# Performance work log

Measured on AMD Instinct MI355X. Metric: run time of the kernel, lower is better.

## Reference

```python
import jax, jax.numpy as jnp
import numpy as np

T, D, E = 65536, 2048, 128
K, G, GLIM = 4, 2, 1  # top-k experts, expert groups, limited groups
TEMP = 1.0
ROUTE_SCALE = 1.0


def setup_inputs() -> dict:
    key = jax.random.key(0)
    kx, kw, kb = jax.random.split(key, 3)
    x = jax.random.normal(kx, (T, D), dtype=jnp.float32)
    # scale router weight so logits have O(1) std (module zero-inits; random here for a non-degenerate test)
    W = jax.random.normal(kw, (E, D), dtype=jnp.float32) * 0.02
    bias = jax.random.normal(kb, (E,), dtype=jnp.float32) * 0.01
    return {"x": x, "W": W, "bias": bias}


def reference(x, W, bias):
    Ttok = x.shape[0]
    gs = E // G  # group size
    logits = x @ W.T + bias                      # [T, E]
    scores = jax.nn.softmax(logits / max(TEMP, 1e-6), axis=-1)
    original_scores = scores
    # group-limited routing (bias is not None -> group rep = sum of top-2 in group)
    scores_g = scores.reshape(Ttok, G, gs)       # [T, G, gs]
    top2 = jax.lax.top_k(scores_g, 2)[0].sum(axis=-1)   # [T, G]
    grp_idx = jax.lax.top_k(top2, GLIM)[1]       # [T, g]
    allow_g = jnp.zeros((Ttok, G), dtype=bool).at[jnp.arange(Ttok)[:, None], grp_idx].set(True)
    allow = jnp.repeat(allow_g, gs, axis=1)      # [T, E]
    masked = jnp.where(allow_g[:, :, None], scores_g, -jnp.inf).reshape(Ttok, E)
    idx = jax.lax.top_k(masked, K)[1]            # [T, k] expert indices
    w = jnp.take_along_axis(original_scores, idx, axis=1)
    w = w / jnp.clip(w.sum(axis=-1, keepdims=True), 1e-9)
    if ROUTE_SCALE != 1.0:
        w = w * ROUTE_SCALE
    return w.astype(x.dtype), idx
```

## Files before the change

### kernel.cpp

```cpp
#include <hip/hip_runtime.h>
#include <math.h>

#define T_TOK 65536
#define D_DIM 2048
#define E_EXP 128
#define K_TOP 4
#define GS    64

#define BM   128
#define BK   32
#define NCH  (D_DIM / BK)
#define LROW 129

#define XSCALE 256.0f
#define WSCALE 256.0f
#define OSCALE (1.0f / 65536.0f)

#define WS_BYTES ((size_t)E_EXP * D_DIM * 2  * 2 )

typedef _Float16 f16x8 __attribute__((ext_vector_type(8)));
typedef float    f32x4 __attribute__((ext_vector_type(4)));
typedef unsigned short u16;

__device__ __forceinline__ void gload_lds16(const void* g, void* l) {
  __builtin_amdgcn_global_load_lds(
      (const __attribute__((address_space(1))) unsigned int*)g,
      (__attribute__((address_space(3))) unsigned int*)l, 16, 0, 0);
}

__global__ __launch_bounds__(256) void prep_w(const float* __restrict__ W,
                                              u16* __restrict__ wsB) {
  const int gid = blockIdx.x * 256 + threadIdx.x;
  const int e   = gid >> 8;
  const int k0  = (gid & 255) << 3;
  const int c   = k0 >> 5;
  const int ks  = (k0 >> 3) & 3;
  const int n16 = e >> 4, r16 = e & 15;
  const float* wp = W + (size_t)e * D_DIM + k0;
  float4 w0 = *(const float4*)(wp);
  float4 w1 = *(const float4*)(wp + 4);
  const float f[8] = {w0.x, w0.y, w0.z, w0.w, w1.x, w1.y, w1.z, w1.w};
  f16x8 hv, lv;
#pragma unroll
  for (int j = 0; j < 8; ++j) {
    float s = f[j] * WSCALE;
    _Float16 h = (_Float16)s;
    hv[j] = h;
    lv[j] = (_Float16)(s - (float)h);
  }
  u16* dst = wsB + (size_t)c * 8192 + (size_t)(n16 * 64 + ks * 16 + r16) * 8;
  *(f16x8*)(dst)        = hv;
  *(f16x8*)(dst + 4096) = lv;
}

template <bool USE_WS>
__global__ __launch_bounds__(256, 2) void gemm_gate(
    const float* __restrict__ x, const float* __restrict__ W,
    const u16* __restrict__ wsB, const float* __restrict__ bias,
    float* __restrict__ w_out, float* __restrict__ idx_out) {
  __shared__ __align__(16) unsigned char smem[BM * LROW * 4];
  __shared__ float bias_lds[E_EXP];
  u16*   As = (u16*)smem;
  u16*   Bs = (u16*)(smem + 16384);
  float* Ls = (float*)smem;

  const int tid = threadIdx.x;
  const int l   = tid & 63;
  const int wid = tid >> 6;
  const int wm  = wid >> 1;
  const int wn  = wid & 1;
  const int lu  = l * 8;

  if (tid < E_EXP) bias_lds[tid] = bias[tid];

  const int row = tid >> 1;
  const int kh  = tid & 1;
  const int m16 = row >> 4, r16 = row & 15;
  const int aw  = (m16 * 64 + kh * 32 + r16) * 8;
  const float* xp = x + (size_t)(blockIdx.x * BM + row) * D_DIM + kh * 16;
  const float* wp = W + (size_t)row * D_DIM + kh * 16;

  f32x4 acc[4][4], sh[4][4];
  const f32x4 vzero = {0.f, 0.f, 0.f, 0.f};
#pragma unroll
  for (int i = 0; i < 4; ++i)
#pragma unroll
    for (int j = 0; j < 4; ++j) { acc[i][j] = vzero; sh[i][j] = vzero; }

  float4 xv0 = *(const float4*)(xp);
  float4 xv1 = *(const float4*)(xp + 4);
  float4 xv2 = *(const float4*)(xp + 8);
  float4 xv3 = *(const float4*)(xp + 12);
  float4 wv0, wv1, wv2, wv3;
  if constexpr (!USE_WS) {
    wv0 = *(const float4*)(wp);
    wv1 = *(const float4*)(wp + 4);
    wv2 = *(const float4*)(wp + 8);
    wv3 = *(const float4*)(wp + 12);
  }

  for (int c = 0; c < NCH; ++c) {
    __syncthreads();

    {
      const float f[16] = {xv0.x, xv0.y, xv0.z, xv0.w, xv1.x, xv1.y, xv1.z, xv1.w,
                           xv2.x, xv2.y, xv2.z, xv2.w, xv3.x, xv3.y, xv3.z, xv3.w};
      f16x8 h0, h1, l0, l1;
#pragma unroll
      for (int j = 0; j < 8; ++j) {
        float sa = f[j] * XSCALE;
        _Float16 ha = (_Float16)sa;
        h0[j] = ha; l0[j] = (_Float16)(sa - (float)ha);
        float sb = f[j + 8] * XSCALE;
        _Float16 hb = (_Float16)sb;
        h1[j] = hb; l1[j] = (_Float16)(sb - (float)hb);
      }
      *(f16x8*)(As + aw)        = h0;
      *(f16x8*)(As + aw + 128)  = h1;
      *(f16x8*)(As + aw + 4096) = l0;
      *(f16x8*)(As + aw + 4224) = l1;
    }

    if constexpr (USE_WS) {
      const u16* src = wsB + (size_t)c * 8192 + tid * 8;
      u16* dst = Bs + tid * 8;
#pragma unroll
      for (int i = 0; i < 4; ++i)
        gload_lds16(src + i * 2048, dst + i * 2048);
    } else {
      const float f[16] = {wv0.x, wv0.y, wv0.z, wv0.w, wv1.x, wv1.y, wv1.z, wv1.w,
                           wv2.x, wv2.y, wv2.z, wv2.w, wv3.x, wv3.y, wv3.z, wv3.w};
      f16x8 h0, h1, l0, l1;
#pragma unroll
      for (int j = 0; j < 8; ++j) {
        float sa = f[j] * WSCALE;
        _Float16 ha = (_Float16)sa;
        h0[j] = ha; l0[j] = (_Float16)(sa - (float)ha);
        float sb = f[j + 8] * WSCALE;
        _Float16 hb = (_Float16)sb;
        h1[j] = hb; l1[j] = (_Float16)(sb - (float)hb);
      }
      *(f16x8*)(Bs + aw)        = h0;
      *(f16x8*)(Bs + aw + 128)  = h1;
      *(f16x8*)(Bs + aw + 4096) = l0;
      *(f16x8*)(Bs + aw + 4224) = l1;
    }

    __syncthreads();

    if (c + 1 < NCH) {
      const float* xn = xp + (c + 1) * 32;
      xv0 = *(const float4*)(xn);
      xv1 = *(const float4*)(xn + 4);
      xv2 = *(const float4*)(xn + 8);
      xv3 = *(const float4*)(xn + 12);
      if constexpr (!USE_WS) {
        const float* wn_ = wp + (c + 1) * 32;
        wv0 = *(const float4*)(wn_);
        wv1 = *(const float4*)(wn_ + 4);
        wv2 = *(const float4*)(wn_ + 8);
        wv3 = *(const float4*)(wn_ + 12);
      }
    }

    f16x8 Ah[4], Al[4];
#pragma unroll
    for (int m_ = 0; m_ < 4; ++m_) {
      const int mt = wm * 4 + m_;
      Ah[m_] = *(const f16x8*)(As + mt * 512 + lu);
      Al[m_] = *(const f16x8*)(As + 4096 + mt * 512 + lu);
    }
#pragma unroll
    for (int n_ = 0; n_ < 4; ++n_) {
      const int nt = wn * 4 + n_;
      f16x8 Bh = *(const f16x8*)(Bs + nt * 512 + lu);
      f16x8 Bl = *(const f16x8*)(Bs + 4096 + nt * 512 + lu);
#pragma unroll
      for (int m_ = 0; m_ < 4; ++m_) {
        acc[m_][n_] = __builtin_amdgcn_mfma_f32_16x16x32_f16(Ah[m_], Bh, acc[m_][n_], 0, 0, 0);
        acc[m_][n_] = __builtin_amdgcn_mfma_f32_16x16x32_f16(Ah[m_], Bl, acc[m_][n_], 0, 0, 0);
        acc[m_][n_] = __builtin_amdgcn_mfma_f32_16x16x32_f16(Al[m_], Bh, acc[m_][n_], 0, 0, 0);
      }
    }

    if ((c & 3) == 3) {
#pragma unroll
      for (int i = 0; i < 4; ++i)
#pragma unroll
        for (int j = 0; j < 4; ++j) { sh[i][j] += acc[i][j]; acc[i][j] = vzero; }
    }
  }

  __syncthreads();

#pragma unroll
  for (int m_ = 0; m_ < 4; ++m_) {
#pragma unroll
    for (int n_ = 0; n_ < 4; ++n_) {
      const int gcol  = wn * 64 + n_ * 16 + (l & 15);
      const int grow0 = wm * 64 + m_ * 16 + ((l >> 4) << 2);
#pragma unroll
      for (int q = 0; q < 4; ++q)
        Ls[(grow0 + q) * LROW + gcol] = sh[m_][n_][q] * OSCALE;
    }
  }
  __syncthreads();

  if (tid < BM) {
    const float* rowp = Ls + tid * LROW;

    float m1[2], m2[2];
#pragma unroll
    for (int g = 0; g < 2; ++g) {
      m1[g] = -INFINITY;
      m2[g] = -INFINITY;
      for (int e = 0; e < GS; ++e) {
        float v = rowp[g * GS + e] + bias_lds[g * GS + e];
        if (v > m1[g]) { m2[g] = m1[g]; m1[g] = v; }
        else if (v > m2[g]) { m2[g] = v; }
      }
    }
    float M  = fmaxf(m1[0], m1[1]);
    float r0 = expf(m1[0] - M) + expf(m2[0] - M);
    float r1 = expf(m1[1] - M) + expf(m2[1] - M);
    int g = (r1 > r0) ? 1 : 0;

    float v4[4] = {-INFINITY, -INFINITY, -INFINITY, -INFINITY};
    int i4[4] = {0, 0, 0, 0};
    const int base = g * GS;
    for (int e = 0; e < GS; ++e) {
      float v = rowp[base + e] + bias_lds[base + e];
      if (v > v4[3]) {
        if (v > v4[1]) {
          if (v > v4[0]) {
            v4[3] = v4[2]; i4[3] = i4[2];
            v4[2] = v4[1]; i4[2] = i4[1];
            v4[1] = v4[0]; i4[1] = i4[0];
            v4[0] = v; i4[0] = e;
          } else {
            v4[3] = v4[2]; i4[3] = i4[2];
            v4[2] = v4[1]; i4[2] = i4[1];
            v4[1] = v; i4[1] = e;
          }
        } else {
          if (v > v4[2]) {
            v4[3] = v4[2]; i4[3] = i4[2];
            v4[2] = v; i4[2] = e;
          } else {
            v4[3] = v; i4[3] = e;
          }
        }
      }
    }

    float s[4], sum = 0.0f;
#pragma unroll
    for (int j = 0; j < 4; ++j) { s[j] = expf(v4[j] - M); sum += s[j]; }
    float denom = fmaxf(sum, 1e-9f);
    const int t = blockIdx.x * BM + tid;
#pragma unroll
    for (int j = 0; j < 4; ++j) {
      w_out[(size_t)t * K_TOP + j]   = s[j] / denom;
      idx_out[(size_t)t * K_TOP + j] = (float)(base + i4[j]);
    }
  }
}

extern "C" void kernel_launch(void* const* d_in, const int* in_sizes, int n_in,
                              void* d_out, int out_size, void* d_ws, size_t ws_size,
                              hipStream_t stream) {
  (void)in_sizes; (void)n_in; (void)out_size;
  const float* x    = (const float*)d_in[0];
  const float* W    = (const float*)d_in[1];
  const float* bias = (const float*)d_in[2];
  float* out = (float*)d_out;

  const bool use_ws = (d_ws != nullptr) && (ws_size >= WS_BYTES);
  if (use_ws) {
    u16* wsB = (u16*)d_ws;
    prep_w<<<E_EXP, 256, 0, stream>>>(W, wsB);
    gemm_gate<true><<<T_TOK / BM, 256, 0, stream>>>(
        x, W, wsB, bias, out, out + (size_t)T_TOK * K_TOP);
  } else {
    gemm_gate<false><<<T_TOK / BM, 256, 0, stream>>>(
        x, W, nullptr, bias, out, out + (size_t)T_TOK * K_TOP);
  }
}
```

Before: 780.8 us.

## Double-buffer LDS tiles to overlap staging with MFMA compute

```diff
diff --git a/kernel.cpp b/kernel.cpp
--- a/kernel.cpp
+++ b/kernel.cpp
@@ -53,6 +53,51 @@
   *(f16x8*)(dst + 4096) = lv;
 }
 
+__device__ __forceinline__ void stage16(u16* dst, int aw, const float4& v0,
+                                        const float4& v1, const float4& v2,
+                                        const float4& v3, float scale) {
+  const float f[16] = {v0.x, v0.y, v0.z, v0.w, v1.x, v1.y, v1.z, v1.w,
+                       v2.x, v2.y, v2.z, v2.w, v3.x, v3.y, v3.z, v3.w};
+  f16x8 h0, h1, l0, l1;
+#pragma unroll
+  for (int j = 0; j < 8; ++j) {
+    float sa = f[j] * scale;
+    _Float16 ha = (_Float16)sa;
+    h0[j] = ha; l0[j] = (_Float16)(sa - (float)ha);
+    float sb = f[j + 8] * scale;
+    _Float16 hb = (_Float16)sb;
+    h1[j] = hb; l1[j] = (_Float16)(sb - (float)hb);
+  }
+  *(f16x8*)(dst + aw)        = h0;
+  *(f16x8*)(dst + aw + 128)  = h1;
+  *(f16x8*)(dst + aw + 4096) = l0;
+  *(f16x8*)(dst + aw + 4224) = l1;
+}
+
+__device__ __forceinline__ void compute32(const u16* As_, const u16* Bs_,
+                                          int wm, int wn, int lu,
+                                          f32x4 (&acc)[4][4]) {
+  f16x8 Ah[4], Al[4];
+#pragma unroll
+  for (int m_ = 0; m_ < 4; ++m_) {
+    const int mt = wm * 4 + m_;
+    Ah[m_] = *(const f16x8*)(As_ + mt * 512 + lu);
+    Al[m_] = *(const f16x8*)(As_ + 4096 + mt * 512 + lu);
+  }
+#pragma unroll
+  for (int n_ = 0; n_ < 4; ++n_) {
+    const int nt = wn * 4 + n_;
+    f16x8 Bh = *(const f16x8*)(Bs_ + nt * 512 + lu);
+    f16x8 Bl = *(const f16x8*)(Bs_ + 4096 + nt * 512 + lu);
+#pragma unroll
+    for (int m_ = 0; m_ < 4; ++m_) {
+      acc[m_][n_] = __builtin_amdgcn_mfma_f32_16x16x32_f16(Ah[m_], Bh, acc[m_][n_], 0, 0, 0);
+      acc[m_][n_] = __builtin_amdgcn_mfma_f32_16x16x32_f16(Ah[m_], Bl, acc[m_][n_], 0, 0, 0);
+      acc[m_][n_] = __builtin_amdgcn_mfma_f32_16x16x32_f16(Al[m_], Bh, acc[m_][n_], 0, 0, 0);
+    }
+  }
+}
+
 template <bool USE_WS>
 __global__ __launch_bounds__(256, 2) void gemm_gate(
     const float* __restrict__ x, const float* __restrict__ W,
@@ -60,8 +105,10 @@
     float* __restrict__ w_out, float* __restrict__ idx_out) {
   __shared__ __align__(16) unsigned char smem[BM * LROW * 4];
   __shared__ float bias_lds[E_EXP];
-  u16*   As = (u16*)smem;
-  u16*   Bs = (u16*)(smem + 16384);
+  u16* As0 = (u16*)smem;
+  u16* As1 = As0 + 8192;
+  u16* Bs0 = As0 + 16384;
+  u16* Bs1 = As0 + 24576;
   float* Ls = (float*)smem;
 
   const int tid = threadIdx.x;
@@ -87,111 +134,87 @@
 #pragma unroll
     for (int j = 0; j < 4; ++j) { acc[i][j] = vzero; sh[i][j] = vzero; }
 
-  float4 xv0 = *(const float4*)(xp);
-  float4 xv1 = *(const float4*)(xp + 4);
-  float4 xv2 = *(const float4*)(xp + 8);
-  float4 xv3 = *(const float4*)(xp + 12);
-  float4 wv0, wv1, wv2, wv3;
-  if constexpr (!USE_WS) {
-    wv0 = *(const float4*)(wp);
-    wv1 = *(const float4*)(wp + 4);
-    wv2 = *(const float4*)(wp + 8);
-    wv3 = *(const float4*)(wp + 12);
-  }
-
-  for (int c = 0; c < NCH; ++c) {
-    __syncthreads();
-
+  float4 xa0, xa1, xa2, xa3, xb0, xb1, xb2, xb3;
+  float4 wa0, wa1, wa2, wa3, wb0, wb1, wb2, wb3;
+
+  {
+    float4 t0 = *(const float4*)(xp);
+    float4 t1 = *(const float4*)(xp + 4);
+    float4 t2 = *(const float4*)(xp + 8);
+    float4 t3 = *(const float4*)(xp + 12);
+    stage16(As0, aw, t0, t1, t2, t3, XSCALE);
+    if constexpr (USE_WS) {
+      const u16* src = wsB + tid * 8;
+#pragma unroll
+      for (int i = 0; i < 4; ++i)
+        gload_lds16(src + i * 2048, Bs0 + tid * 8 + i * 2048);
+    } else {
+      float4 s0 = *(const float4*)(wp);
+      float4 s1 = *(const float4*)(wp + 4);
+      float4 s2 = *(const float4*)(wp + 8);
+      float4 s3 = *(const float4*)(wp + 12);
+      stage16(Bs0, aw, s0, s1, s2, s3, WSCALE);
+    }
+    const float* xn = xp + BK;
+    xb0 = *(const float4*)(xn);      xb1 = *(const float4*)(xn + 4);
+    xb2 = *(const float4*)(xn + 8);  xb3 = *(const float4*)(xn + 12);
+    if constexpr (!USE_WS) {
+      const float* wn_ = wp + BK;
+      wb0 = *(const float4*)(wn_);      wb1 = *(const float4*)(wn_ + 4);
+      wb2 = *(const float4*)(wn_ + 8);  wb3 = *(const float4*)(wn_ + 12);
+    }
+  }
+  __syncthreads();
+
+  for (int c = 0; c < NCH; c += 2) {
     {
-      const float f[16] = {xv0.x, xv0.y, xv0.z, xv0.w, xv1.x, xv1.y, xv1.z, xv1.w,
-                           xv2.x, xv2.y, xv2.z, xv2.w, xv3.x, xv3.y, xv3.z, xv3.w};
-      f16x8 h0, h1, l0, l1;
-#pragma unroll
-      for (int j = 0; j < 8; ++j) {
-        float sa = f[j] * XSCALE;
-        _Float16 ha = (_Float16)sa;
-        h0[j] = ha; l0[j] = (_Float16)(sa - (float)ha);
-        float sb = f[j + 8] * XSCALE;
-        _Float16 hb = (_Float16)sb;
-        h1[j] = hb; l1[j] = (_Float16)(sb - (float)hb);
-      }
-      *(f16x8*)(As + aw)        = h0;
-      *(f16x8*)(As + aw + 128)  = h1;
-      *(f16x8*)(As + aw + 4096) = l0;
-      *(f16x8*)(As + aw + 4224) = l1;
-    }
-
-    if constexpr (USE_WS) {
-      const u16* src = wsB + (size_t)c * 8192 + tid * 8;
-      u16* dst = Bs + tid * 8;
-#pragma unroll
-      for (int i = 0; i < 4; ++i)
-        gload_lds16(src + i * 2048, dst + i * 2048);
-    } else {
-      const float f[16] = {wv0.x, wv0.y, wv0.z, wv0.w, wv1.x, wv1.y, wv1.z, wv1.w,
-                           wv2.x, wv2.y, wv2.z, wv2.w, wv3.x, wv3.y, wv3.z, wv3.w};
-      f16x8 h0, h1, l0, l1;
-#pragma unroll
-      for (int j = 0; j < 8; ++j) {
-        float sa = f[j] * WSCALE;
-        _Float16 ha = (_Float16)sa;
-        h0[j] = ha; l0[j] = (_Float16)(sa - (float)ha);
-        float sb = f[j + 8] * WSCALE;
-        _Float16 hb = (_Float16)sb;
-        h1[j] = hb; l1[j] = (_Float16)(sb - (float)hb);
-      }
-      *(f16x8*)(Bs + aw)        = h0;
-      *(f16x8*)(Bs + aw + 128)  = h1;
-      *(f16x8*)(Bs + aw + 4096) = l0;
-      *(f16x8*)(Bs + aw + 4224) = l1;
-    }
-
-    __syncthreads();
-
-    if (c + 1 < NCH) {
-      const float* xn = xp + (c + 1) * 32;
-      xv0 = *(const float4*)(xn);
-      xv1 = *(const float4*)(xn + 4);
-      xv2 = *(const float4*)(xn + 8);
-      xv3 = *(const float4*)(xn + 12);
-      if constexpr (!USE_WS) {
-        const float* wn_ = wp + (c + 1) * 32;
-        wv0 = *(const float4*)(wn_);
-        wv1 = *(const float4*)(wn_ + 4);
-        wv2 = *(const float4*)(wn_ + 8);
-        wv3 = *(const float4*)(wn_ + 12);
-      }
-    }
-
-    f16x8 Ah[4], Al[4];
-#pragma unroll
-    for (int m_ = 0; m_ < 4; ++m_) {
-      const int mt = wm * 4 + m_;
-      Ah[m_] = *(const f16x8*)(As + mt * 512 + lu);
-      Al[m_] = *(const f16x8*)(As + 4096 + mt * 512 + lu);
-    }
-#pragma unroll
-    for (int n_ = 0; n_ < 4; ++n_) {
-      const int nt = wn * 4 + n_;
-      f16x8 Bh = *(const f16x8*)(Bs + nt * 512 + lu);
-      f16x8 Bl = *(const f16x8*)(Bs + 4096 + nt * 512 + lu);
-#pragma unroll
-      for (int m_ = 0; m_ < 4; ++m_) {
-        acc[m_][n_] = __builtin_amdgcn_mfma_f32_16x16x32_f16(Ah[m_], Bh, acc[m_][n_], 0, 0, 0);
-        acc[m_][n_] = __builtin_amdgcn_mfma_f32_16x16x32_f16(Ah[m_], Bl, acc[m_][n_], 0, 0, 0);
-        acc[m_][n_] = __builtin_amdgcn_mfma_f32_16x16x32_f16(Al[m_], Bh, acc[m_][n_], 0, 0, 0);
-      }
-    }
-
-    if ((c & 3) == 3) {
-#pragma unroll
-      for (int i = 0; i < 4; ++i)
-#pragma unroll
-        for (int j = 0; j < 4; ++j) { sh[i][j] += acc[i][j]; acc[i][j] = vzero; }
-    }
-  }
-
-  __syncthreads();
+      const int cn = (c + 2 < NCH) ? c + 2 : NCH - 1;
+      const float* xn = xp + cn * BK;
+      xa0 = *(const float4*)(xn);      xa1 = *(const float4*)(xn + 4);
+      xa2 = *(const float4*)(xn + 8);  xa3 = *(const float4*)(xn + 12);
+      if constexpr (USE_WS) {
+        const u16* src = wsB + (size_t)(c + 1) * 8192 + tid * 8;
+#pragma unroll
+        for (int i = 0; i < 4; ++i)
+          gload_lds16(src + i * 2048, Bs1 + tid * 8 + i * 2048);
+      } else {
+        const float* wn_ = wp + cn * BK;
+        wa0 = *(const float4*)(wn_);      wa1 = *(const float4*)(wn_ + 4);
+        wa2 = *(const float4*)(wn_ + 8);  wa3 = *(const float4*)(wn_ + 12);
+        stage16(Bs1, aw, wb0, wb1, wb2, wb3, WSCALE);
+      }
+      stage16(As1, aw, xb0, xb1, xb2, xb3, XSCALE);
+      compute32(As0, Bs0, wm, wn, lu, acc);
+      __syncthreads();
+    }
+    {
+      const int cs = (c + 2 < NCH) ? c + 2 : NCH - 1;
+      const int cl = (c + 3 < NCH) ? c + 3 : NCH - 1;
+      const float* xn = xp + cl * BK;
+      xb0 = *(const float4*)(xn);      xb1 = *(const float4*)(xn + 4);
+      xb2 = *(const float4*)(xn + 8);  xb3 = *(const float4*)(xn + 12);
+      if constexpr (USE_WS) {
+        const u16* src = wsB + (size_t)cs * 8192 + tid * 8;
+#pragma unroll
+        for (int i = 0; i < 4; ++i)
+          gload_lds16(src + i * 2048, Bs0 + tid * 8 + i * 2048);
+      } else {
+        const float* wn_ = wp + cl * BK;
+        wb0 = *(const float4*)(wn_);      wb1 = *(const float4*)(wn_ + 4);
+        wb2 = *(const float4*)(wn_ + 8);  wb3 = *(const float4*)(wn_ + 12);
+        stage16(Bs0, aw, wa0, wa1, wa2, wa3, WSCALE);
+      }
+      stage16(As0, aw, xa0, xa1, xa2, xa3, XSCALE);
+      compute32(As1, Bs1, wm, wn, lu, acc);
+      if (((c + 1) & 3) == 3) {
+#pragma unroll
+        for (int i = 0; i < 4; ++i)
+#pragma unroll
+          for (int j = 0; j < 4; ++j) { sh[i][j] += acc[i][j]; acc[i][j] = vzero; }
+      }
+      __syncthreads();
+    }
+  }
 
 #pragma unroll
   for (int m_ = 0; m_ < 4; ++m_) {
```

Measured after the change: 768.3 us. No clear change (-1.6%).
